# Performance work log

Hardware: AMD Instinct MI355X
Metric: run time of the kernel (lower is better)

The kernel has to match this reference:

```python
import jax, jax.numpy as jnp
import numpy as np

EMB = 1024
HEADS = 16
DK = EMB // HEADS
EPS = 1e-5


def setup_inputs() -> dict:
    key = jax.random.key(0)
    ks = jax.random.split(key, 7)
    s_in = 1.0 / np.sqrt(EMB)
    return {
        "x": jax.random.normal(ks[0], (4, 2048, EMB), dtype=jnp.float32),
        "W_qkv": jax.random.uniform(ks[1], (EMB, 3 * EMB), jnp.float32, -s_in, s_in),
        "b_qkv": jax.random.uniform(ks[2], (3 * EMB,), jnp.float32, -s_in, s_in),
        "W_out": jax.random.uniform(ks[3], (EMB, EMB), jnp.float32, -s_in, s_in),
        "b_out": jax.random.uniform(ks[4], (EMB,), jnp.float32, -s_in, s_in),
        "gamma": jnp.ones((EMB,), jnp.float32),
        "beta": jnp.zeros((EMB,), jnp.float32),
    }


def reference(x, W_qkv, b_qkv, W_out, b_out, gamma, beta):
    B, T, D = x.shape
    qkv = x @ W_qkv + b_qkv                      # [B,T,3D]
    q, k, v = jnp.split(qkv, 3, axis=-1)
    # [B,T,D] -> [B,H,T,dk]
    def heads(t):
        return t.reshape(B, T, HEADS, DK).transpose(0, 2, 1, 3)
    q, k, v = heads(q), heads(k), heads(v)
    scores = jnp.einsum("bhtd,bhsd->bhts", q, k) / np.sqrt(DK)
    attn = jax.nn.softmax(scores, axis=-1)
    out = jnp.einsum("bhts,bhsd->bhtd", attn, v)  # [B,H,T,dk]
    out = out.transpose(0, 2, 1, 3).reshape(B, T, D)
    out = out @ W_out + b_out
    res = x + out
    mu = jnp.mean(res, axis=-1, keepdims=True)
    var = jnp.mean((res - mu) ** 2, axis=-1, keepdims=True)
    return (res - mu) / jnp.sqrt(var + EPS) * gamma + beta
```

## Files before the change

### kernel.cpp

```cpp
#include <hip/hip_runtime.h>

#define B_ 4
#define T_ 2048
#define D_ 1024
#define H_ 16
#define DK_ 64
#define M_ (B_*T_)

typedef __bf16 bf16;
typedef __bf16 bf16x8 __attribute__((ext_vector_type(8)));
typedef __bf16 bf16x4 __attribute__((ext_vector_type(4)));
typedef short s16x4 __attribute__((ext_vector_type(4)));
typedef float f32x4 __attribute__((ext_vector_type(4)));

__device__ __forceinline__ f32x4 zero4() { f32x4 v = {0.f, 0.f, 0.f, 0.f}; return v; }

__device__ __forceinline__ float fexp2(float x) {
  float r;
  asm("v_exp_f32 %0, %1\n\ts_nop 0" : "=v"(r) : "v"(x));
  return r;
}

__device__ __forceinline__ float max3f(float a, float b, float c) {
  float r;
  asm("v_max3_f32 %0, %1, %2, %3" : "=v"(r) : "v"(a), "v"(b), "v"(c));
  return r;
}

__device__ __forceinline__ void g2l16(const void* g, void* l) {
  __builtin_amdgcn_global_load_lds(
      (const __attribute__((address_space(1))) void*)g,
      (__attribute__((address_space(3))) void*)l, 16, 0, 0);
}

__global__ __launch_bounds__(256) void cast_bf16(const float* __restrict__ src,
                                                 bf16* __restrict__ dst) {
  const size_t i = ((size_t)blockIdx.x * 256 + threadIdx.x) * 8;
  float4 a = *(const float4*)(src + i);
  float4 b = *(const float4*)(src + i + 4);
  bf16x8 v;
  v[0] = (bf16)a.x; v[1] = (bf16)a.y; v[2] = (bf16)a.z; v[3] = (bf16)a.w;
  v[4] = (bf16)b.x; v[5] = (bf16)b.y; v[6] = (bf16)b.z; v[7] = (bf16)b.w;
  *(bf16x8*)(dst + i) = v;
}

__global__ __launch_bounds__(256) void transpose_wf(const float* __restrict__ src,
                                                    bf16* __restrict__ dst, int R, int C) {
  __shared__ alignas(16) bf16 ts[64 * 65];
  const int tid = threadIdx.x;
  const int r0 = blockIdx.x * 64, c0 = blockIdx.y * 64;
  {
    int rr = tid >> 2, cc = (tid & 3) * 16;
    const float4* p4 = (const float4*)(src + (size_t)(r0 + rr) * C + c0 + cc);
    float fv[16];
#pragma unroll
    for (int q = 0; q < 4; ++q) *(float4*)&fv[q * 4] = p4[q];
#pragma unroll
    for (int i = 0; i < 16; ++i) ts[(cc + i) * 65 + rr] = (bf16)fv[i];
  }
  __syncthreads();
  {
    int rr = tid >> 2, cc = (tid & 3) * 16;
    bf16x8 a, b;
#pragma unroll
    for (int i = 0; i < 8; ++i) a[i] = ts[rr * 65 + cc + i];
#pragma unroll
    for (int i = 0; i < 8; ++i) b[i] = ts[rr * 65 + cc + 8 + i];
    bf16* q = dst + (size_t)(c0 + rr) * R + r0 + cc;
    *(bf16x8*)q = a;
    *(bf16x8*)(q + 8) = b;
  }
}

__global__ __launch_bounds__(256) void transpose_v(const bf16* __restrict__ qkv,
                                                   bf16* __restrict__ Vt) {
  __shared__ alignas(16) bf16 ts[64 * 65];
  int bid = blockIdx.x;
  const int tt = bid & 31; bid >>= 5;
  const int h = bid & 15;  const int b = bid >> 4;
  const int t0 = tt * 64;
  const int tid = threadIdx.x;
  {
    int tok = tid >> 2, fc = (tid & 3) * 16;
    const bf16* p = qkv + (size_t)(b * T_ + t0 + tok) * (3 * D_) + 2 * D_ + h * DK_ + fc;
    bf16x8 a = *(const bf16x8*)p;
    bf16x8 c = *(const bf16x8*)(p + 8);
#pragma unroll
    for (int i = 0; i < 8; ++i) ts[(fc + i) * 65 + tok] = a[i];
#pragma unroll
    for (int i = 0; i < 8; ++i) ts[(fc + 8 + i) * 65 + tok] = c[i];
  }
  __syncthreads();
  {
    int f = tid >> 2, tc = (tid & 3) * 16;
    bf16x8 a, c;
#pragma unroll
    for (int i = 0; i < 8; ++i) a[i] = ts[f * 65 + tc + i];
#pragma unroll
    for (int i = 0; i < 8; ++i) c[i] = ts[f * 65 + tc + 8 + i];
    bf16* q = Vt + ((size_t)(b * H_ + h) * DK_ + f) * T_ + t0 + tc;
    *(bf16x8*)q = a;
    *(bf16x8*)(q + 8) = c;
  }
}

template <int ASRC, bool FUSE>
__global__ __launch_bounds__(256) void gemm128(const void* __restrict__ Av,
                                               const bf16* __restrict__ Bt,
                                               const float* __restrict__ bias,
                                               bf16* __restrict__ Cbf,
                                               float* __restrict__ Cf,
                                               const float* __restrict__ resid,
                                               int N, int K, int lda, int ldc) {
  __shared__ alignas(16) bf16 As[128 * 32];
  __shared__ alignas(16) bf16 Bs[128 * 32];
  const int tid = threadIdx.x;
  const int wid = tid >> 6, lane = tid & 63, quad = lane >> 4, l16 = lane & 15;
  const int m0 = blockIdx.x * 128, n0 = blockIdx.y * 128;
  const int wr = (wid >> 1) * 64, wc = (wid & 1) * 64;

  f32x4 acc[4][4];
#pragma unroll
  for (int i = 0; i < 4; ++i)
#pragma unroll
    for (int j = 0; j < 4; ++j) acc[i][j] = zero4();

  for (int k0 = 0; k0 < K; k0 += 32) {
    bf16x8 ar[2];
    if (ASRC == 0) {
#pragma unroll
      for (int p = 0; p < 2; ++p) {
        int t = p * 256 + tid;
        int row = t >> 2, kc = (t & 3) * 8;
        const float* ap = (const float*)Av + (size_t)(m0 + row) * lda + k0 + kc;
        float4 a0 = *(const float4*)ap, a1 = *(const float4*)(ap + 4);
        bf16x8 v;
        v[0] = (bf16)a0.x; v[1] = (bf16)a0.y; v[2] = (bf16)a0.z; v[3] = (bf16)a0.w;
        v[4] = (bf16)a1.x; v[5] = (bf16)a1.y; v[6] = (bf16)a1.z; v[7] = (bf16)a1.w;
        ar[p] = v;
      }
    }
    __syncthreads();
#pragma unroll
    for (int p = 0; p < 2; ++p) {
      int t = p * 256 + tid;
      int row = t >> 2, kc = (t & 3) * 8;
      g2l16(Bt + (size_t)(n0 + row) * K + k0 + kc, (char*)Bs + p * 4096 + wid * 1024);
      if (ASRC == 1)
        g2l16((const bf16*)Av + (size_t)(m0 + row) * lda + k0 + kc,
              (char*)As + p * 4096 + wid * 1024);
      else
        *(bf16x8*)&As[row * 32 + kc] = ar[p];
    }
    __syncthreads();
    bf16x8 af[4], bfr[4];
#pragma unroll
    for (int i = 0; i < 4; ++i)
      af[i] = *(const bf16x8*)&As[(wr + i * 16 + l16) * 32 + quad * 8];
#pragma unroll
    for (int j = 0; j < 4; ++j)
      bfr[j] = *(const bf16x8*)&Bs[(wc + j * 16 + l16) * 32 + quad * 8];
#pragma unroll
    for (int i = 0; i < 4; ++i)
#pragma unroll
      for (int j = 0; j < 4; ++j)
        acc[i][j] = __builtin_amdgcn_mfma_f32_16x16x32_bf16(af[i], bfr[j], acc[i][j], 0, 0, 0);
  }

#pragma unroll
  for (int i = 0; i < 4; ++i) {
#pragma unroll
    for (int j = 0; j < 4; ++j) {
      const int col = n0 + wc + j * 16 + l16;
      const float bv = bias[col];
#pragma unroll
      for (int r = 0; r < 4; ++r) {
        const int row = m0 + wr + i * 16 + quad * 4 + r;
        const float v = acc[i][j][r] + bv;
        if (FUSE) {
          const size_t off = (size_t)row * N + col;
          Cf[off] = v + resid[off];
        } else {
          Cbf[(size_t)row * ldc + col] = (bf16)v;
        }
      }
    }
  }
}

__global__ __launch_bounds__(256, 4) void attn_db(const bf16* __restrict__ qkv,
                                                  const bf16* __restrict__ Vt,
                                                  bf16* __restrict__ out) {
  __shared__ alignas(16) bf16 Ks[2][64 * 64];
  __shared__ alignas(16) bf16 Vs[2][64 * 64];
  const int tid = threadIdx.x;
  const int wid = tid >> 6, lane = tid & 63, quad = lane >> 4, l16 = lane & 15;
  const int bid = blockIdx.x;
  const int qb = bid & 15, h = (bid >> 4) & 15, b = bid >> 8;
  const int q0 = qb * 128;

  const int lrow8 = lane >> 3;
  const int kch = (lane & 7) ^ lrow8;
  const bf16* kg = qkv + (size_t)(b * T_ + wid * 16 + lrow8) * (3 * D_) + D_ + h * DK_ + kch * 8;
  const bf16* vg = Vt + ((size_t)(b * H_ + h) * DK_ + wid * 16 + lrow8) * T_ + kch * 8;

  const float SC = 0.125f * 1.44269504f;
  bf16x8 qA[2], qB[2];
  {
    const bf16* qpA = qkv + (size_t)(b * T_ + q0 + wid * 32 + l16) * (3 * D_) + h * DK_ + quad * 8;
    const bf16* qpB = qpA + (size_t)16 * (3 * D_);
    qA[0] = *(const bf16x8*)qpA;       qA[1] = *(const bf16x8*)(qpA + 32);
    qB[0] = *(const bf16x8*)qpB;       qB[1] = *(const bf16x8*)(qpB + 32);
#pragma unroll
    for (int i = 0; i < 8; ++i) {
      qA[0][i] = (bf16)((float)qA[0][i] * SC); qA[1][i] = (bf16)((float)qA[1][i] * SC);
      qB[0][i] = (bf16)((float)qB[0][i] * SC); qB[1][i] = (bf16)((float)qB[1][i] * SC);
    }
  }

  float miA = -1e30f, liA = 0.f, miB = -1e30f, liB = 0.f;
  f32x4 oA[4], oB[4];
#pragma unroll
  for (int ft = 0; ft < 4; ++ft) { oA[ft] = zero4(); oB[ft] = zero4(); }

  auto stage = [&](int buf, int t0) {
    g2l16(kg + (size_t)(t0 + 0) * (3 * D_), &Ks[buf][(wid * 16 + 0) * 64]);
    g2l16(kg + (size_t)(t0 + 8) * (3 * D_), &Ks[buf][(wid * 16 + 8) * 64]);
    g2l16(vg + (size_t)0 * T_ + t0,         &Vs[buf][(wid * 16 + 0) * 64]);
    g2l16(vg + (size_t)8 * T_ + t0,         &Vs[buf][(wid * 16 + 8) * 64]);
  };

  stage(0, 0);
  __syncthreads();

  for (int kt = 0; kt < T_ / 64; ++kt) {
    const int cur = kt & 1;
    if (kt + 1 < T_ / 64) stage(cur ^ 1, (kt + 1) * 64);

    f32x4 svA[4], svB[4];
#pragma unroll
    for (int nt = 0; nt < 4; ++nt) { svA[nt] = zero4(); svB[nt] = zero4(); }
    __builtin_amdgcn_s_setprio(1);
#pragma unroll
    for (int nt = 0; nt < 4; ++nt)
#pragma unroll
      for (int ks = 0; ks < 2; ++ks) {
        const bf16x8 kf = *(const bf16x8*)
            &Ks[cur][(nt * 16 + l16) * 64 + (((ks << 2) | quad) ^ (l16 & 7)) * 8];
        svA[nt] = __builtin_amdgcn_mfma_f32_16x16x32_bf16(kf, qA[ks], svA[nt], 0, 0, 0);
        svB[nt] = __builtin_amdgcn_mfma_f32_16x16x32_bf16(kf, qB[ks], svB[nt], 0, 0, 0);
      }
    __builtin_amdgcn_s_setprio(0);

    float a0 = max3f(svA[0][0], svA[0][1], svA[0][2]);
    float a1 = max3f(svA[0][3], svA[1][0], svA[1][1]);
    a0 = max3f(a0, svA[1][2], svA[1][3]);
    a1 = max3f(a1, svA[2][0], svA[2][1]);
    a0 = max3f(a0, svA[2][2], svA[2][3]);
    a1 = max3f(a1, svA[3][0], svA[3][1]);
    a0 = max3f(a0, svA[3][2], svA[3][3]);
    float b0 = max3f(svB[0][0], svB[0][1], svB[0][2]);
    float b1 = max3f(svB[0][3], svB[1][0], svB[1][1]);
    b0 = max3f(b0, svB[1][2], svB[1][3]);
    b1 = max3f(b1, svB[2][0], svB[2][1]);
    b0 = max3f(b0, svB[2][2], svB[2][3]);
    b1 = max3f(b1, svB[3][0], svB[3][1]);
    b0 = max3f(b0, svB[3][2], svB[3][3]);
    float tA = fmaxf(a0, a1), tB = fmaxf(b0, b1);
    tA = fmaxf(tA, __shfl_xor(tA, 16, 64));
    tA = fmaxf(tA, __shfl_xor(tA, 32, 64));
    tB = fmaxf(tB, __shfl_xor(tB, 16, 64));
    tB = fmaxf(tB, __shfl_xor(tB, 32, 64));

    if (!__all(tA <= miA + 8.f)) {
      const float nm = fmaxf(miA, tA);
      const float al = fexp2(miA - nm);
      miA = nm; liA *= al;
#pragma unroll
      for (int r = 0; r < 4; ++r) {
        const float ar = __shfl(al, quad * 4 + r, 64);
#pragma unroll
        for (int ft = 0; ft < 4; ++ft) oA[ft][r] *= ar;
      }
    }
    if (!__all(tB <= miB + 8.f)) {
      const float nm = fmaxf(miB, tB);
      const float al = fexp2(miB - nm);
      miB = nm; liB *= al;
#pragma unroll
      for (int r = 0; r < 4; ++r) {
        const float ar = __shfl(al, quad * 4 + r, 64);
#pragma unroll
        for (int ft = 0; ft < 4; ++ft) oB[ft][r] *= ar;
      }
    }

    s16x4 pA[4], pB[4];
    f32x4 s4A = zero4(), s4B = zero4();
#pragma unroll
    for (int nt = 0; nt < 4; ++nt) {
      f32x4 dA = svA[nt] - miA;
      dA[0] = fexp2(dA[0]); dA[1] = fexp2(dA[1]); dA[2] = fexp2(dA[2]); dA[3] = fexp2(dA[3]);
      s4A += dA;
      union { bf16x4 b; s16x4 s; } ua;
#pragma unroll
      for (int j = 0; j < 4; ++j) ua.b[j] = (bf16)dA[j];
      pA[nt] = ua.s;
      f32x4 dB = svB[nt] - miB;
      dB[0] = fexp2(dB[0]); dB[1] = fexp2(dB[1]); dB[2] = fexp2(dB[2]); dB[3] = fexp2(dB[3]);
      s4B += dB;
      union { bf16x4 b; s16x4 s; } ub;
#pragma unroll
      for (int j = 0; j < 4; ++j) ub.b[j] = (bf16)dB[j];
      pB[nt] = ub.s;
    }
    float sA = (s4A[0] + s4A[1]) + (s4A[2] + s4A[3]);
    float sB = (s4B[0] + s4B[1]) + (s4B[2] + s4B[3]);
    sA += __shfl_xor(sA, 16, 64);
    sA += __shfl_xor(sA, 32, 64);
    sB += __shfl_xor(sB, 16, 64);
    sB += __shfl_xor(sB, 32, 64);
    liA += sA; liB += sB;

    __builtin_amdgcn_s_setprio(1);
#pragma unroll
    for (int ks = 0; ks < 4; ++ks)
#pragma unroll
      for (int ft = 0; ft < 4; ++ft) {
        const s16x4 vf = *(const s16x4*)
            &Vs[cur][(ft * 16 + l16) * 64 +
                     ((ks * 2 + (quad >> 1)) ^ (l16 & 7)) * 8 + (quad & 1) * 4];
        oA[ft] = __builtin_amdgcn_mfma_f32_16x16x16bf16_1k(pA[ks], vf, oA[ft], 0, 0, 0);
        oB[ft] = __builtin_amdgcn_mfma_f32_16x16x16bf16_1k(pB[ks], vf, oB[ft], 0, 0, 0);
      }
    __builtin_amdgcn_s_setprio(0);

    __syncthreads();
  }

#pragma unroll
  for (int r = 0; r < 4; ++r) {
    const float invA = 1.0f / __shfl(liA, quad * 4 + r, 64);
    const float invB = 1.0f / __shfl(liB, quad * 4 + r, 64);
    const int rowA = b * T_ + q0 + wid * 32 + quad * 4 + r;
    const int rowB = rowA + 16;
#pragma unroll
    for (int ft = 0; ft < 4; ++ft) {
      out[(size_t)rowA * (3 * D_) + h * DK_ + ft * 16 + l16] = (bf16)(oA[ft][r] * invA);
      out[(size_t)rowB * (3 * D_) + h * DK_ + ft * 16 + l16] = (bf16)(oB[ft][r] * invB);
    }
  }
}

__global__ __launch_bounds__(256) void ln_out(float* __restrict__ res,
                                              const float* __restrict__ gamma,
                                              const float* __restrict__ beta) {
  const int row = blockIdx.x * 4 + (threadIdx.x >> 6);
  const int lane = threadIdx.x & 63;
  float4 v[4];
  float s = 0.f, q = 0.f;
#pragma unroll
  for (int p = 0; p < 4; ++p) {
    v[p] = *(const float4*)(res + (size_t)row * D_ + p * 256 + lane * 4);
    s += v[p].x + v[p].y + v[p].z + v[p].w;
    q += v[p].x * v[p].x + v[p].y * v[p].y + v[p].z * v[p].z + v[p].w * v[p].w;
  }
#pragma unroll
  for (int m = 1; m < 64; m <<= 1) { s += __shfl_xor(s, m, 64); q += __shfl_xor(q, m, 64); }
  const float mu = s * (1.0f / D_);
  const float var = q * (1.0f / D_) - mu * mu;
  const float rstd = rsqrtf(var + 1e-5f);
#pragma unroll
  for (int p = 0; p < 4; ++p) {
    const int c = p * 256 + lane * 4;
    const float4 g = *(const float4*)(gamma + c);
    const float4 be = *(const float4*)(beta + c);
    float4 ov;
    ov.x = (v[p].x - mu) * rstd * g.x + be.x;
    ov.y = (v[p].y - mu) * rstd * g.y + be.y;
    ov.z = (v[p].z - mu) * rstd * g.z + be.z;
    ov.w = (v[p].w - mu) * rstd * g.w + be.w;
    *(float4*)(res + (size_t)row * D_ + c) = ov;
  }
}

extern "C" void kernel_launch(void* const* d_in, const int* in_sizes, int n_in,
                              void* d_out, int out_size, void* d_ws, size_t ws_size,
                              hipStream_t stream) {
  const float* x     = (const float*)d_in[0];
  const float* Wqkv  = (const float*)d_in[1];
  const float* bqkv  = (const float*)d_in[2];
  const float* Wout  = (const float*)d_in[3];
  const float* bout  = (const float*)d_in[4];
  const float* gamma = (const float*)d_in[5];
  const float* beta  = (const float*)d_in[6];
  float* out = (float*)d_out;

  char* ws = (char*)d_ws;
  bf16* WqkvT = (bf16*)ws; ws += (size_t)3 * D_ * D_ * 2;
  bf16* WoutT = (bf16*)ws; ws += (size_t)D_ * D_ * 2;
  bf16* qkv   = (bf16*)ws; ws += (size_t)M_ * 3 * D_ * 2;
  bf16* Vt    = (bf16*)ws;
  bf16* attn  = qkv + 2 * D_;
  bf16* xb    = Vt;

  transpose_wf<<<dim3(D_ / 64, 3 * D_ / 64), 256, 0, stream>>>(Wqkv, WqkvT, D_, 3 * D_);
  transpose_wf<<<dim3(D_ / 64, D_ / 64), 256, 0, stream>>>(Wout, WoutT, D_, D_);
  cast_bf16<<<M_ * D_ / (256 * 8), 256, 0, stream>>>(x, xb);
  gemm128<1, false><<<dim3(M_ / 128, 3 * D_ / 128), 256, 0, stream>>>(
      xb, WqkvT, bqkv, qkv, nullptr, nullptr, 3 * D_, D_, D_, 3 * D_);
  transpose_v<<<B_ * H_ * (T_ / 64), 256, 0, stream>>>(qkv, Vt);
  attn_db<<<B_ * H_ * (T_ / 128), 256, 0, stream>>>(qkv, Vt, attn);
  gemm128<1, true><<<dim3(M_ / 128, D_ / 128), 256, 0, stream>>>(
      attn, WoutT, bout, nullptr, out, x, D_, D_, 3 * D_, D_);
  ln_out<<<M_ / 4, 256, 0, stream>>>(out, gamma, beta);
}
```

Measured before the change: 330.5 us.

## Widen GEMM K-tile to 64 with XOR-swizzled LDS and defer softmax row sums

The GEMM kernel now stages a K=64 slice per iteration with an XOR swizzle on the LDS column chunks. This halves the number of barrier pairs per K loop and avoids LDS bank conflicts on the fragment reads. The unused fp32 A-source path is removed. In attention, the per-lane partial row sums are kept in a vector and reduced across lanes once at the end instead of every tile, and the max shuffle reduction now runs only when a rescale is needed. The larger tile doubles LDS use per block, which may lower occupancy.

```diff
diff --git a/kernel.cpp b/kernel.cpp
--- a/kernel.cpp
+++ b/kernel.cpp
@@ -104,20 +104,21 @@
   }
 }
 
-template <int ASRC, bool FUSE>
-__global__ __launch_bounds__(256) void gemm128(const void* __restrict__ Av,
-                                               const bf16* __restrict__ Bt,
-                                               const float* __restrict__ bias,
-                                               bf16* __restrict__ Cbf,
-                                               float* __restrict__ Cf,
-                                               const float* __restrict__ resid,
-                                               int N, int K, int lda, int ldc) {
-  __shared__ alignas(16) bf16 As[128 * 32];
-  __shared__ alignas(16) bf16 Bs[128 * 32];
+template <bool FUSE>
+__global__ __launch_bounds__(256) void gemm64(const bf16* __restrict__ A,
+                                              const bf16* __restrict__ Bt,
+                                              const float* __restrict__ bias,
+                                              bf16* __restrict__ Cbf,
+                                              float* __restrict__ Cf,
+                                              const float* __restrict__ resid,
+                                              int N, int K, int lda, int ldc) {
+  __shared__ alignas(16) bf16 As[128 * 64];
+  __shared__ alignas(16) bf16 Bs[128 * 64];
   const int tid = threadIdx.x;
   const int wid = tid >> 6, lane = tid & 63, quad = lane >> 4, l16 = lane & 15;
   const int m0 = blockIdx.x * 128, n0 = blockIdx.y * 128;
   const int wr = (wid >> 1) * 64, wc = (wid & 1) * 64;
+  const int sw = l16 & 7;
 
   f32x4 acc[4][4];
 #pragma unroll
@@ -125,46 +126,32 @@
 #pragma unroll
     for (int j = 0; j < 4; ++j) acc[i][j] = zero4();
 
-  for (int k0 = 0; k0 < K; k0 += 32) {
-    bf16x8 ar[2];
-    if (ASRC == 0) {
-#pragma unroll
-      for (int p = 0; p < 2; ++p) {
-        int t = p * 256 + tid;
-        int row = t >> 2, kc = (t & 3) * 8;
-        const float* ap = (const float*)Av + (size_t)(m0 + row) * lda + k0 + kc;
-        float4 a0 = *(const float4*)ap, a1 = *(const float4*)(ap + 4);
-        bf16x8 v;
-        v[0] = (bf16)a0.x; v[1] = (bf16)a0.y; v[2] = (bf16)a0.z; v[3] = (bf16)a0.w;
-        v[4] = (bf16)a1.x; v[5] = (bf16)a1.y; v[6] = (bf16)a1.z; v[7] = (bf16)a1.w;
-        ar[p] = v;
-      }
-    }
+  for (int k0 = 0; k0 < K; k0 += 64) {
     __syncthreads();
 #pragma unroll
-    for (int p = 0; p < 2; ++p) {
-      int t = p * 256 + tid;
-      int row = t >> 2, kc = (t & 3) * 8;
-      g2l16(Bt + (size_t)(n0 + row) * K + k0 + kc, (char*)Bs + p * 4096 + wid * 1024);
-      if (ASRC == 1)
-        g2l16((const bf16*)Av + (size_t)(m0 + row) * lda + k0 + kc,
-              (char*)As + p * 4096 + wid * 1024);
-      else
-        *(bf16x8*)&As[row * 32 + kc] = ar[p];
+    for (int p = 0; p < 4; ++p) {
+      const int t = p * 256 + tid;
+      const int row = t >> 3;
+      const int kcs = ((t & 7) ^ (row & 7)) * 8;
+      g2l16(Bt + (size_t)(n0 + row) * K + k0 + kcs, (char*)Bs + p * 4096 + wid * 1024);
+      g2l16(A + (size_t)(m0 + row) * lda + k0 + kcs, (char*)As + p * 4096 + wid * 1024);
     }
     __syncthreads();
-    bf16x8 af[4], bfr[4];
-#pragma unroll
-    for (int i = 0; i < 4; ++i)
-      af[i] = *(const bf16x8*)&As[(wr + i * 16 + l16) * 32 + quad * 8];
-#pragma unroll
-    for (int j = 0; j < 4; ++j)
-      bfr[j] = *(const bf16x8*)&Bs[(wc + j * 16 + l16) * 32 + quad * 8];
-#pragma unroll
-    for (int i = 0; i < 4; ++i)
+#pragma unroll
+    for (int kk = 0; kk < 2; ++kk) {
+      bf16x8 af[4], bfr[4];
+#pragma unroll
+      for (int i = 0; i < 4; ++i)
+        af[i] = *(const bf16x8*)&As[(wr + i * 16 + l16) * 64 + ((((kk << 2) | quad) ^ sw) * 8)];
 #pragma unroll
       for (int j = 0; j < 4; ++j)
-        acc[i][j] = __builtin_amdgcn_mfma_f32_16x16x32_bf16(af[i], bfr[j], acc[i][j], 0, 0, 0);
+        bfr[j] = *(const bf16x8*)&Bs[(wc + j * 16 + l16) * 64 + ((((kk << 2) | quad) ^ sw) * 8)];
+#pragma unroll
+      for (int i = 0; i < 4; ++i)
+#pragma unroll
+        for (int j = 0; j < 4; ++j)
+          acc[i][j] = __builtin_amdgcn_mfma_f32_16x16x32_bf16(af[i], bfr[j], acc[i][j], 0, 0, 0);
+    }
   }
 
 #pragma unroll
@@ -218,7 +205,8 @@
     }
   }
 
-  float miA = -1e30f, liA = 0.f, miB = -1e30f, liB = 0.f;
+  float miA = -1e30f, miB = -1e30f;
+  f32x4 liA4 = zero4(), liB4 = zero4();
   f32x4 oA[4], oB[4];
 #pragma unroll
   for (int ft = 0; ft < 4; ++ft) { oA[ft] = zero4(); oB[ft] = zero4(); }
@@ -266,16 +254,14 @@
     b0 = max3f(b0, svB[2][2], svB[2][3]);
     b1 = max3f(b1, svB[3][0], svB[3][1]);
     b0 = max3f(b0, svB[3][2], svB[3][3]);
-    float tA = fmaxf(a0, a1), tB = fmaxf(b0, b1);
-    tA = fmaxf(tA, __shfl_xor(tA, 16, 64));
-    tA = fmaxf(tA, __shfl_xor(tA, 32, 64));
-    tB = fmaxf(tB, __shfl_xor(tB, 16, 64));
-    tB = fmaxf(tB, __shfl_xor(tB, 32, 64));
-
-    if (!__all(tA <= miA + 8.f)) {
+    const float tAl = fmaxf(a0, a1), tBl = fmaxf(b0, b1);
+
+    if (!__all(tAl <= miA + 8.f)) {
+      float tA = fmaxf(tAl, __shfl_xor(tAl, 16, 64));
+      tA = fmaxf(tA, __shfl_xor(tA, 32, 64));
       const float nm = fmaxf(miA, tA);
       const float al = fexp2(miA - nm);
-      miA = nm; liA *= al;
+      miA = nm; liA4 *= al;
 #pragma unroll
       for (int r = 0; r < 4; ++r) {
         const float ar = __shfl(al, quad * 4 + r, 64);
@@ -283,10 +269,12 @@
         for (int ft = 0; ft < 4; ++ft) oA[ft][r] *= ar;
       }
     }
-    if (!__all(tB <= miB + 8.f)) {
+    if (!__all(tBl <= miB + 8.f)) {
+      float tB = fmaxf(tBl, __shfl_xor(tBl, 16, 64));
+      tB = fmaxf(tB, __shfl_xor(tB, 32, 64));
       const float nm = fmaxf(miB, tB);
       const float al = fexp2(miB - nm);
-      miB = nm; liB *= al;
+      miB = nm; liB4 *= al;
 #pragma unroll
       for (int r = 0; r < 4; ++r) {
         const float ar = __shfl(al, quad * 4 + r, 64);
@@ -296,31 +284,23 @@
     }
 
     s16x4 pA[4], pB[4];
-    f32x4 s4A = zero4(), s4B = zero4();
 #pragma unroll
     for (int nt = 0; nt < 4; ++nt) {
       f32x4 dA = svA[nt] - miA;
       dA[0] = fexp2(dA[0]); dA[1] = fexp2(dA[1]); dA[2] = fexp2(dA[2]); dA[3] = fexp2(dA[3]);
-      s4A += dA;
+      liA4 += dA;
       union { bf16x4 b; s16x4 s; } ua;
 #pragma unroll
       for (int j = 0; j < 4; ++j) ua.b[j] = (bf16)dA[j];
       pA[nt] = ua.s;
       f32x4 dB = svB[nt] - miB;
       dB[0] = fexp2(dB[0]); dB[1] = fexp2(dB[1]); dB[2] = fexp2(dB[2]); dB[3] = fexp2(dB[3]);
-      s4B += dB;
+      liB4 += dB;
       union { bf16x4 b; s16x4 s; } ub;
 #pragma unroll
       for (int j = 0; j < 4; ++j) ub.b[j] = (bf16)dB[j];
       pB[nt] = ub.s;
     }
-    float sA = (s4A[0] + s4A[1]) + (s4A[2] + s4A[3]);
-    float sB = (s4B[0] + s4B[1]) + (s4B[2] + s4B[3]);
-    sA += __shfl_xor(sA, 16, 64);
-    sA += __shfl_xor(sA, 32, 64);
-    sB += __shfl_xor(sB, 16, 64);
-    sB += __shfl_xor(sB, 32, 64);
-    liA += sA; liB += sB;
 
     __builtin_amdgcn_s_setprio(1);
 #pragma unroll
@@ -338,10 +318,17 @@
     __syncthreads();
   }
 
+  float sA = (liA4[0] + liA4[1]) + (liA4[2] + liA4[3]);
+  sA += __shfl_xor(sA, 16, 64);
+  sA += __shfl_xor(sA, 32, 64);
+  float sB = (liB4[0] + liB4[1]) + (liB4[2] + liB4[3]);
+  sB += __shfl_xor(sB, 16, 64);
+  sB += __shfl_xor(sB, 32, 64);
+
 #pragma unroll
   for (int r = 0; r < 4; ++r) {
-    const float invA = 1.0f / __shfl(liA, quad * 4 + r, 64);
-    const float invB = 1.0f / __shfl(liB, quad * 4 + r, 64);
+    const float invA = 1.0f / __shfl(sA, quad * 4 + r, 64);
+    const float invB = 1.0f / __shfl(sB, quad * 4 + r, 64);
     const int rowA = b * T_ + q0 + wid * 32 + quad * 4 + r;
     const int rowB = rowA + 16;
 #pragma unroll
@@ -407,11 +394,11 @@
   transpose_wf<<<dim3(D_ / 64, 3 * D_ / 64), 256, 0, stream>>>(Wqkv, WqkvT, D_, 3 * D_);
   transpose_wf<<<dim3(D_ / 64, D_ / 64), 256, 0, stream>>>(Wout, WoutT, D_, D_);
   cast_bf16<<<M_ * D_ / (256 * 8), 256, 0, stream>>>(x, xb);
-  gemm128<1, false><<<dim3(M_ / 128, 3 * D_ / 128), 256, 0, stream>>>(
+  gemm64<false><<<dim3(M_ / 128, 3 * D_ / 128), 256, 0, stream>>>(
       xb, WqkvT, bqkv, qkv, nullptr, nullptr, 3 * D_, D_, D_, 3 * D_);
   transpose_v<<<B_ * H_ * (T_ / 64), 256, 0, stream>>>(qkv, Vt);
   attn_db<<<B_ * H_ * (T_ / 128), 256, 0, stream>>>(qkv, Vt, attn);
-  gemm128<1, true><<<dim3(M_ / 128, D_ / 128), 256, 0, stream>>>(
+  gemm64<true><<<dim3(M_ / 128, D_ / 128), 256, 0, stream>>>(
       attn, WoutT, bout, nullptr, out, x, D_, D_, 3 * D_, D_);
   ln_out<<<M_ / 4, 256, 0, stream>>>(out, gamma, beta);
 }
```

Measured after the change: 307.5 us. -7.0%, faster.
